# Performance work log

Hardware: AMD Instinct MI355X
Metric: run time of the kernel (lower is better)

## Reference

```python
import jax, jax.numpy as jnp
import numpy as np

N = 100000   # nodes
M = 200000   # gathered (combined-subgraph) node entries
E = 600000   # combined-subgraph edges
B = 128      # graphs
P = 32       # patches per graph (METIS)
BP = B * P
DIN = 64; H = 256; RW = 16
L = 4        # GCN layers
LM = 4       # mixer layers
T = 64       # token-mixing hidden dim
CH = 4 * H   # channel-mixing hidden dim
DOUT = 10


def _seg_mean(v, idx, n):
    s = jax.ops.segment_sum(v, idx, num_segments=n)
    c = jax.ops.segment_sum(jnp.ones((v.shape[0],), v.dtype), idx, num_segments=n)
    return s / jnp.maximum(c, 1.0)[:, None]


def _ln(x, s, b):
    m = jnp.mean(x, -1, keepdims=True)
    v = jnp.var(x, -1, keepdims=True)
    return (x - m) * jax.lax.rsqrt(v + 1e-5) * s + b


def setup_inputs() -> dict:
    key = jax.random.key(0)
    ks = jax.random.split(key, 40)
    w = lambda k, s: jax.random.normal(k, s, jnp.float32) * 0.02
    inp = {
        'x': jax.random.normal(ks[0], (N, DIN), jnp.float32),
        'patch_pe': jax.random.normal(ks[1], (BP, RW), jnp.float32),
        'mask': jnp.ones((B, P), jnp.bool_),
        'nodes_mapper': jax.random.randint(ks[2], (M,), 0, N),
        'subgraphs_batch': jnp.sort(jax.random.randint(ks[3], (M,), 0, BP)),
        'edge_index': jax.random.randint(ks[4], (2, E), 0, M),
        # pre_mp
        'W_pre': w(ks[5], (DIN, H)), 'b_pre': jnp.zeros((H,), jnp.float32),
        # U MLPs (layers-1 of them) and GCN weights
        'W_u': w(ks[6], (L - 1, H, H)), 'b_u': jnp.zeros((L - 1, H), jnp.float32),
        'W_g': w(ks[7], (L, H, H)), 'b_g': jnp.zeros((L, H), jnp.float32),
        # patch RW-PE 2-layer MLP
        'Wp1': w(ks[8], (RW, H)), 'bp1': jnp.zeros((H,), jnp.float32),
        'Wp2': w(ks[9], (H, H)), 'bp2': jnp.zeros((H,), jnp.float32),
        # MLPMixer blocks (stacked over LM layers)
        'ln1_s': jnp.ones((LM, H), jnp.float32), 'ln1_b': jnp.zeros((LM, H), jnp.float32),
        'Wt1': w(ks[10], (LM, P, T)), 'bt1': jnp.zeros((LM, T), jnp.float32),
        'Wt2': w(ks[11], (LM, T, P)), 'bt2': jnp.zeros((LM, P), jnp.float32),
        'ln2_s': jnp.ones((LM, H), jnp.float32), 'ln2_b': jnp.zeros((LM, H), jnp.float32),
        'Wc1': w(ks[12], (LM, H, CH)), 'bc1': jnp.zeros((LM, CH), jnp.float32),
        'Wc2': w(ks[13], (LM, CH, H)), 'bc2': jnp.zeros((LM, H), jnp.float32),
        # head
        'ln_f_s': jnp.ones((H,), jnp.float32), 'ln_f_b': jnp.zeros((H,), jnp.float32),
        'W_head': w(ks[14], (H, DOUT)), 'b_head': jnp.zeros((DOUT,), jnp.float32),
    }
    return inp


def reference(x, patch_pe, mask, nodes_mapper, subgraphs_batch, edge_index,
              W_pre, b_pre, W_u, b_u, W_g, b_g, Wp1, bp1, Wp2, bp2,
              ln1_s, ln1_b, Wt1, bt1, Wt2, bt2, ln2_s, ln2_b, Wc1, bc1, Wc2, bc2,
              ln_f_s, ln_f_b, W_head, b_head):
    # pre_mp: linear + relu on node features [N, H]
    h = jax.nn.relu(x @ W_pre + b_pre)
    # gather nodes into combined-subgraph space [M, H]
    h = h[nodes_mapper]
    src, dst = edge_index[0], edge_index[1]
    # GCN symmetric normalization with self loops (degree over M-space)
    deg = jax.ops.segment_sum(jnp.ones((src.shape[0],), h.dtype), dst, num_segments=M) + 1.0
    nrm = jax.lax.rsqrt(deg)
    edge_nrm = (nrm[src] * nrm[dst])[:, None]
    self_nrm = (nrm * nrm)[:, None]
    for i in range(L):
        if i > 0:
            # pre_layer_scatter: pool per subgraph, broadcast back, add U-MLP
            sub = _seg_mean(h, subgraphs_batch, BP)[subgraphs_batch]
            h = h + jax.nn.relu(sub @ W_u[i - 1] + b_u[i - 1])
            # post_layer_scatter: mean over duplicated nodes, broadcast back
            h = _seg_mean(h, nodes_mapper, N)[nodes_mapper]
        # GCNConv + relu
        hw = h @ W_g[i]
        agg = jax.ops.segment_sum(hw[src] * edge_nrm, dst, num_segments=M)
        h = jax.nn.relu(agg + hw * self_nrm + b_g[i])
    # final_scatter: pool to [B*P, H]
    h = _seg_mean(h, subgraphs_batch, BP)
    # patch random-walk PE encoder (2-layer MLP) added
    pe = jax.nn.relu(jax.nn.relu(patch_pe @ Wp1 + bp1) @ Wp2 + bp2)
    z = (h + pe).reshape(B, P, H)
    # MLPMixer
    for l in range(LM):
        y = jnp.swapaxes(_ln(z, ln1_s[l], ln1_b[l]), 1, 2)  # [B, H, P]
        y = jax.nn.gelu(y @ Wt1[l] + bt1[l]) @ Wt2[l] + bt2[l]
        z = z + jnp.swapaxes(y, 1, 2)
        y = _ln(z, ln2_s[l], ln2_b[l])
        z = z + (jax.nn.gelu(y @ Wc1[l] + bc1[l]) @ Wc2[l] + bc2[l])
    # masked mean pooling over patches
    m = mask.astype(z.dtype)
    g = (z * m[:, :, None]).sum(1) / m.sum(1, keepdims=True)
    # head
    g = _ln(g, ln_f_s, ln_f_b)
    return g @ W_head + b_head
```

## Files before the change

### kernel.cpp

```cpp
#include <hip/hip_runtime.h>
#include <math.h>

namespace {

typedef unsigned short u16;
typedef unsigned int u32;
typedef unsigned long long u64;
typedef __attribute__((ext_vector_type(8))) short bf16x8;
typedef __attribute__((ext_vector_type(8))) unsigned short u16x8;
typedef __attribute__((ext_vector_type(4))) float f32x4;

constexpr int kN = 100000, kM = 200000, kE = 600000;
constexpr int kB = 128, kP = 32, kBP = kB * kP;
constexpr int kDIN = 64, kH = 256, kRW = 16;
constexpr int kL = 4, kLM = 4, kT = 64, kCH = 4 * kH, kDOUT = 10;
constexpr int kScanCB = 1024;

__device__ __forceinline__ float geluf(float x) {
  const float c = 0.7978845608028654f;
  float x3 = x * x * x;
  return 0.5f * x * (1.f + tanhf(c * (x + 0.044715f * x3)));
}

__device__ __forceinline__ float bf2f(u16 h) {
  u32 u = ((u32)h) << 16;
  return __uint_as_float(u);
}
__device__ __forceinline__ u16 f2bf(float f) {
  u32 u = __float_as_uint(f);
  u32 r = (u + 0x7FFFu + ((u >> 16) & 1u)) >> 16;
  return (u16)r;
}
__device__ __forceinline__ float4 bf4_to_f4(ushort4 v) {
  return make_float4(bf2f(v.x), bf2f(v.y), bf2f(v.z), bf2f(v.w));
}
__device__ __forceinline__ ushort4 f4_to_bf4(float4 v) {
  ushort4 r;
  r.x = f2bf(v.x); r.y = f2bf(v.y); r.z = f2bf(v.z); r.w = f2bf(v.w);
  return r;
}

template <int RPT>
__global__ __launch_bounds__(256) void k_gemm(
    const float* __restrict__ A, const float* __restrict__ B,
    const float* __restrict__ bias, const float* __restrict__ res,
    float* __restrict__ C, int Mr, int Nc, int Kc, int act) {
  constexpr int BM = 16 * RPT;
  __shared__ float As[16][BM];
  __shared__ float Bs[16][64];
  int tid = threadIdx.x;
  int tx = tid & 15, ty = tid >> 4;
  int bm = blockIdx.x * BM, bn = blockIdx.y * 64;
  float acc[RPT][4];
#pragma unroll
  for (int i = 0; i < RPT; ++i)
#pragma unroll
    for (int j = 0; j < 4; ++j) acc[i][j] = 0.f;

  for (int k0 = 0; k0 < Kc; k0 += 16) {
#pragma unroll
    for (int l = 0; l < RPT / 4; ++l) {
      int idx = tid + l * 256;
      int r = idx >> 2, c4 = (idx & 3) * 4;
      float4 a4 = make_float4(0.f, 0.f, 0.f, 0.f);
      if (bm + r < Mr) a4 = *(const float4*)(A + (size_t)(bm + r) * Kc + k0 + c4);
      As[c4 + 0][r] = a4.x; As[c4 + 1][r] = a4.y;
      As[c4 + 2][r] = a4.z; As[c4 + 3][r] = a4.w;
    }
    {
      int kr = tid >> 4, cc = (tid & 15) * 4;
      float4 b4 = *(const float4*)(B + (size_t)(k0 + kr) * Nc + bn + cc);
      *(float4*)&Bs[kr][cc] = b4;
    }
    __syncthreads();
#pragma unroll
    for (int k = 0; k < 16; ++k) {
      float a[RPT], bb[4];
#pragma unroll
      for (int l = 0; l < RPT / 4; ++l) {
        float4 av = *(const float4*)&As[k][ty * RPT + l * 4];
        a[l * 4 + 0] = av.x; a[l * 4 + 1] = av.y;
        a[l * 4 + 2] = av.z; a[l * 4 + 3] = av.w;
      }
      float4 bv = *(const float4*)&Bs[k][tx * 4];
      bb[0] = bv.x; bb[1] = bv.y; bb[2] = bv.z; bb[3] = bv.w;
#pragma unroll
      for (int i = 0; i < RPT; ++i)
#pragma unroll
        for (int j = 0; j < 4; ++j) acc[i][j] = fmaf(a[i], bb[j], acc[i][j]);
    }
    __syncthreads();
  }
#pragma unroll
  for (int i = 0; i < RPT; ++i) {
    int row = bm + ty * RPT + i;
    if (row >= Mr) continue;
#pragma unroll
    for (int j = 0; j < 4; ++j) {
      int col = bn + tx * 4 + j;
      float v = acc[i][j];
      if (bias) v += bias[col];
      if (act == 1) v = fmaxf(v, 0.f);
      else if (act == 2) v = geluf(v);
      if (res) v += res[(size_t)row * Nc + col];
      C[(size_t)row * Nc + col] = v;
    }
  }
}

__global__ void k_packw(const float* __restrict__ W, u16* __restrict__ Wp,
                        int KB, int NC, int L) {
  int per = KB * NC * 16 * 64;
  int o8 = blockIdx.x * 256 + threadIdx.x;
  if (o8 >= L * per) return;
  int li = o8 / per, r = o8 % per;
  int l = r & 63;
  int t = r >> 6;
  int nt = t & 15, q = t >> 4;
  int kbg = q % KB, nc = q / KB;
  int Kc = KB * 32, Ncols = NC * 256;
  int col = nc * 256 + nt * 16 + (l & 15);
  int k0 = kbg * 32 + (l >> 4) * 8;
  const float* w = W + (size_t)li * Kc * Ncols;
  u16* o = Wp + (size_t)o8 * 8;
#pragma unroll
  for (int i = 0; i < 8; ++i) o[i] = f2bf(w[(size_t)(k0 + i) * Ncols + col]);
}

__global__ __launch_bounds__(256) void k_gemm_rowblk_mfma(
    const u16* A, const u16* __restrict__ Wp, u16* C, int Mr) {
  __shared__ u16 As[64 * 256];
  __shared__ u16 Bs[8192];
  int tid = threadIdx.x;
  int w = tid >> 6, l = tid & 63;
  int bm = blockIdx.x * 64;
  u16x8 pre[4];
#pragma unroll
  for (int j = 0; j < 4; ++j) pre[j] = *(const u16x8*)(Wp + tid * 8 + j * 2048);
#pragma unroll
  for (int i = 0; i < 8; ++i) {
    int idx = tid + i * 256;
    int row = idx >> 5, seg = idx & 31;
    u16x8 v = (u16x8){0, 0, 0, 0, 0, 0, 0, 0};
    if (bm + row < Mr) v = *(const u16x8*)(A + (size_t)(bm + row) * 256 + seg * 8);
    *(u16x8*)((char*)As + row * 512 + ((seg * 16) ^ ((row & 15) << 4))) = v;
  }

  f32x4 acc[16];
#pragma unroll
  for (int nt = 0; nt < 16; ++nt) acc[nt] = (f32x4){0.f, 0.f, 0.f, 0.f};
  int a_row = w * 16 + (l & 15);
  int a_xor = (a_row & 15) << 4;
  for (int kb = 0; kb < 8; ++kb) {
    __syncthreads();
#pragma unroll
    for (int j = 0; j < 4; ++j) *(u16x8*)(Bs + tid * 8 + j * 2048) = pre[j];
    __syncthreads();
    if (kb < 7) {
#pragma unroll
      for (int j = 0; j < 4; ++j)
        pre[j] = *(const u16x8*)(Wp + (kb + 1) * 8192 + tid * 8 + j * 2048);
    }
    int abyte = a_row * 512 + ((kb * 64 + (l >> 4) * 16) ^ a_xor);
    bf16x8 af = *(const bf16x8*)((const char*)As + abyte);
#pragma unroll
    for (int nt = 0; nt < 16; ++nt) {
      bf16x8 bf = *(const bf16x8*)(Bs + nt * 512 + l * 8);
      acc[nt] = __builtin_amdgcn_mfma_f32_16x16x32_bf16(af, bf, acc[nt], 0, 0, 0);
    }
  }
  __syncthreads();
  int c_row0 = w * 16 + (l >> 4) * 4;
  int ccol = l & 15;
#pragma unroll
  for (int nt = 0; nt < 16; ++nt) {
#pragma unroll
    for (int j = 0; j < 4; ++j) {
      int row = c_row0 + j;
      int colbyte = (nt * 16 + ccol) * 2;
      *(u16*)((char*)As + row * 512 + (colbyte ^ ((row & 15) << 4))) = f2bf(acc[nt][j]);
    }
  }
  __syncthreads();
#pragma unroll
  for (int i = 0; i < 8; ++i) {
    int idx = tid + i * 256;
    int row = idx >> 5, seg = idx & 31;
    if (bm + row < Mr) {
      u16x8 v = *(const u16x8*)((const char*)As + row * 512 + ((seg * 16) ^ ((row & 15) << 4)));
      *(u16x8*)(C + (size_t)(bm + row) * 256 + seg * 8) = v;
    }
  }
}

__global__ __launch_bounds__(256) void k_gemm_mfma_s(
    const void* __restrict__ Av, const u16* __restrict__ Wp,
    const float* __restrict__ bias, const float* __restrict__ res,
    void* __restrict__ Cv, int Kc, int Ncols, int act, int outw, int abf, int kclen) {
  __shared__ u16 As[64 * 256];
  __shared__ u16 Bs[8192];
  int tid = threadIdx.x;
  int w = tid >> 6, l = tid & 63;
  int bm = blockIdx.x * 64;
  int nchunk = blockIdx.y, bn = nchunk * 256;
  int kcs = blockIdx.z * kclen;
  int KB = Kc >> 5;
  const u16* wseq = Wp + (size_t)nchunk * KB * 8192;

  u16x8 pre[4];
#pragma unroll
  for (int j = 0; j < 4; ++j)
    pre[j] = *(const u16x8*)(wseq + (size_t)(kcs >> 5) * 8192 + tid * 8 + j * 2048);

  f32x4 acc[16];
#pragma unroll
  for (int nt = 0; nt < 16; ++nt) acc[nt] = (f32x4){0.f, 0.f, 0.f, 0.f};
  int a_row = w * 16 + (l & 15);
  int a_xor = (a_row & 15) << 4;

  for (int kc0 = kcs; kc0 < kcs + kclen; kc0 += 256) {
    __syncthreads();
#pragma unroll
    for (int i = 0; i < 8; ++i) {
      int idx = tid + i * 256;
      int row = idx >> 5, seg = idx & 31;
      u16x8 hv;
      if (abf) {
        hv = *(const u16x8*)((const u16*)Av + (size_t)(bm + row) * Kc + kc0 + seg * 8);
      } else {
        const float* s = (const float*)Av + (size_t)(bm + row) * Kc + kc0 + seg * 8;
        float4 v0 = *(const float4*)s;
        float4 v1 = *(const float4*)(s + 4);
        hv[0] = f2bf(v0.x); hv[1] = f2bf(v0.y); hv[2] = f2bf(v0.z); hv[3] = f2bf(v0.w);
        hv[4] = f2bf(v1.x); hv[5] = f2bf(v1.y); hv[6] = f2bf(v1.z); hv[7] = f2bf(v1.w);
      }
      *(u16x8*)((char*)As + row * 512 + ((seg * 16) ^ ((row & 15) << 4))) = hv;
    }
    int kbg0 = kc0 >> 5;
    for (int kb = 0; kb < 8; ++kb) {
      int t = kbg0 + kb;
      __syncthreads();
#pragma unroll
      for (int j = 0; j < 4; ++j) *(u16x8*)(Bs + tid * 8 + j * 2048) = pre[j];
      __syncthreads();
      if (t + 1 < KB) {
#pragma unroll
        for (int j = 0; j < 4; ++j)
          pre[j] = *(const u16x8*)(wseq + (size_t)(t + 1) * 8192 + tid * 8 + j * 2048);
      }
      int abyte = a_row * 512 + ((kb * 64 + (l >> 4) * 16) ^ a_xor);
      bf16x8 af = *(const bf16x8*)((const char*)As + abyte);
#pragma unroll
      for (int nt = 0; nt < 16; ++nt) {
        bf16x8 bf = *(const bf16x8*)(Bs + nt * 512 + l * 8);
        acc[nt] = __builtin_amdgcn_mfma_f32_16x16x32_bf16(af, bf, acc[nt], 0, 0, 0);
      }
    }
  }

  int c_row0 = w * 16 + (l >> 4) * 4;
  int ccol = l & 15;
  if (outw == 2) {
    float* C = (float*)Cv;
    bool addb = (kcs == 0);
#pragma unroll
    for (int nt = 0; nt < 16; ++nt) {
      int col = bn + nt * 16 + ccol;
      float bv = addb ? bias[col] : 0.f;
#pragma unroll
      for (int j = 0; j < 4; ++j) {
        int row = bm + c_row0 + j;
        atomicAdd(&C[(size_t)row * Ncols + col], acc[nt][j] + bv);
      }
    }
  } else if (outw == 1) {
    float* C = (float*)Cv;
#pragma unroll
    for (int nt = 0; nt < 16; ++nt) {
      int col = bn + nt * 16 + ccol;
      float bv = bias[col];
#pragma unroll
      for (int j = 0; j < 4; ++j) {
        int row = bm + c_row0 + j;
        float v = acc[nt][j] + bv;
        if (act == 1) v = fmaxf(v, 0.f);
        else if (act == 2) v = geluf(v);
        if (res) v += res[(size_t)row * Ncols + col];
        C[(size_t)row * Ncols + col] = v;
      }
    }
  } else {
    u16* C = (u16*)Cv;
    __syncthreads();
#pragma unroll
    for (int nt = 0; nt < 16; ++nt) {
      float bv = bias[bn + nt * 16 + ccol];
#pragma unroll
      for (int j = 0; j < 4; ++j) {
        int row = c_row0 + j;
        float v = acc[nt][j] + bv;
        if (act == 1) v = fmaxf(v, 0.f);
        else if (act == 2) v = geluf(v);
        int colbyte = (nt * 16 + ccol) * 2;
        *(u16*)((char*)As + row * 512 + (colbyte ^ ((row & 15) << 4))) = f2bf(v);
      }
    }
    __syncthreads();
#pragma unroll
    for (int i = 0; i < 8; ++i) {
      int idx = tid + i * 256;
      int row = idx >> 5, seg = idx & 31;
      u16x8 v = *(const u16x8*)((const char*)As + row * 512 + ((seg * 16) ^ ((row & 15) << 4)));
      *(u16x8*)(C + (size_t)(bm + row) * Ncols + bn + seg * 8) = v;
    }
  }
}

__global__ __launch_bounds__(256) void k_premp_mfma(
    const float* __restrict__ A, const u16* __restrict__ Wp,
    const float* __restrict__ bias, u16* __restrict__ C, int Mr) {
  __shared__ u16 As[64 * 256];
  __shared__ u16 Bs[8192];
  int tid = threadIdx.x;
  int w = tid >> 6, l = tid & 63;
  int bm = blockIdx.x * 64;
  u16x8 pre[4];
#pragma unroll
  for (int j = 0; j < 4; ++j) pre[j] = *(const u16x8*)(Wp + tid * 8 + j * 2048);
#pragma unroll
  for (int i = 0; i < 2; ++i) {
    int idx = tid + i * 256;
    int row = idx >> 3, seg = idx & 7;
    u16x8 hv = (u16x8){0, 0, 0, 0, 0, 0, 0, 0};
    if (bm + row < Mr) {
      const float* s = A + (size_t)(bm + row) * 64 + seg * 8;
      float4 v0 = *(const float4*)s;
      float4 v1 = *(const float4*)(s + 4);
      hv[0] = f2bf(v0.x); hv[1] = f2bf(v0.y); hv[2] = f2bf(v0.z); hv[3] = f2bf(v0.w);
      hv[4] = f2bf(v1.x); hv[5] = f2bf(v1.y); hv[6] = f2bf(v1.z); hv[7] = f2bf(v1.w);
    }
    *(u16x8*)((char*)As + row * 128 + ((seg * 16) ^ ((row & 7) << 4))) = hv;
  }

  f32x4 acc[16];
#pragma unroll
  for (int nt = 0; nt < 16; ++nt) acc[nt] = (f32x4){0.f, 0.f, 0.f, 0.f};
  int a_row = w * 16 + (l & 15);
#pragma unroll
  for (int kb = 0; kb < 2; ++kb) {
    __syncthreads();
#pragma unroll
    for (int j = 0; j < 4; ++j) *(u16x8*)(Bs + tid * 8 + j * 2048) = pre[j];
    __syncthreads();
    if (kb == 0) {
#pragma unroll
      for (int j = 0; j < 4; ++j)
        pre[j] = *(const u16x8*)(Wp + 8192 + tid * 8 + j * 2048);
    }
    int abyte = a_row * 128 + ((kb * 64 + (l >> 4) * 16) ^ ((a_row & 7) << 4));
    bf16x8 af = *(const bf16x8*)((const char*)As + abyte);
#pragma unroll
    for (int nt = 0; nt < 16; ++nt) {
      bf16x8 bf = *(const bf16x8*)(Bs + nt * 512 + l * 8);
      acc[nt] = __builtin_amdgcn_mfma_f32_16x16x32_bf16(af, bf, acc[nt], 0, 0, 0);
    }
  }
  __syncthreads();
  int c_row0 = w * 16 + (l >> 4) * 4;
  int ccol = l & 15;
#pragma unroll
  for (int nt = 0; nt < 16; ++nt) {
    float bv = bias[nt * 16 + ccol];
#pragma unroll
    for (int j = 0; j < 4; ++j) {
      int row = c_row0 + j;
      float v = fmaxf(acc[nt][j] + bv, 0.f);
      int colbyte = (nt * 16 + ccol) * 2;
      *(u16*)((char*)As + row * 512 + (colbyte ^ ((row & 15) << 4))) = f2bf(v);
    }
  }
  __syncthreads();
#pragma unroll
  for (int i = 0; i < 8; ++i) {
    int idx = tid + i * 256;
    int row = idx >> 5, seg = idx & 31;
    if (bm + row < Mr) {
      u16x8 v = *(const u16x8*)((const char*)As + row * 512 + ((seg * 16) ^ ((row & 15) << 4)));
      *(u16x8*)(C + (size_t)(bm + row) * 256 + seg * 8) = v;
    }
  }
}

__global__ void k_hist(const int* __restrict__ idx, int* __restrict__ cnt, int n) {
  int i = blockIdx.x * 256 + threadIdx.x;
  if (i < n) atomicAdd(&cnt[idx[i]], 1);
}

__global__ __launch_bounds__(256) void k_scan_a(const int* __restrict__ cnt, int n,
                                                int* __restrict__ bsum) {
  __shared__ int red[256];
  int b = blockIdx.x, t = threadIdx.x;
  int base = b * kScanCB + t * 4;
  int s = 0;
#pragma unroll
  for (int j = 0; j < 4; ++j) { int i = base + j; if (i < n) s += cnt[i]; }
  red[t] = s;
  __syncthreads();
  for (int d = 128; d; d >>= 1) {
    if (t < d) red[t] += red[t + d];
    __syncthreads();
  }
  if (t == 0) bsum[b] = red[0];
}

__global__ __launch_bounds__(256) void k_scan_b(const int* __restrict__ bsum, int G,
                                                int* __restrict__ boff,
                                                int* __restrict__ total_out) {
  __shared__ int sd[256];
  int t = threadIdx.x;
  sd[t] = (t < G) ? bsum[t] : 0;
  __syncthreads();
  for (int d = 1; d < 256; d <<= 1) {
    int u = (t >= d) ? sd[t - d] : 0;
    __syncthreads();
    sd[t] += u;
    __syncthreads();
  }
  if (t < G) boff[t] = t ? sd[t - 1] : 0;
  if (t == 255) *total_out = sd[255];
}

__global__ __launch_bounds__(256) void k_scan_c(const int* __restrict__ cnt, int n,
                                                const int* __restrict__ boff,
                                                int* __restrict__ out) {
  __shared__ int sd[256];
  int b = blockIdx.x, t = threadIdx.x;
  int base = b * kScanCB + t * 4;
  int c[4];
  int s = 0;
#pragma unroll
  for (int j = 0; j < 4; ++j) {
    int i = base + j;
    c[j] = (i < n) ? cnt[i] : 0;
    s += c[j];
  }
  sd[t] = s;
  __syncthreads();
  for (int d = 1; d < 256; d <<= 1) {
    int u = (t >= d) ? sd[t - d] : 0;
    __syncthreads();
    sd[t] += u;
    __syncthreads();
  }
  int run = boff[b] + (t ? sd[t - 1] : 0);
#pragma unroll
  for (int j = 0; j < 4; ++j) {
    int i = base + j;
    if (i < n) out[i] = run;
    run += c[j];
  }
}

__global__ void k_nrm(const int* __restrict__ cnt, float* __restrict__ nrm, int n) {
  int i = blockIdx.x * 256 + threadIdx.x;
  if (i < n) nrm[i] = rsqrtf((float)cnt[i] + 1.f);
}

__global__ void k_scatter_e(const int* __restrict__ src, const int* __restrict__ dst,
                            const int* __restrict__ nmap, const float* __restrict__ nrm,
                            const int* __restrict__ rs, int* __restrict__ cur,
                            int* __restrict__ gidx, float* __restrict__ w) {
  int e = blockIdx.x * 256 + threadIdx.x;
  if (e >= kE) return;
  int s = src[e], d = dst[e];
  int p = rs[d] + atomicAdd(&cur[d], 1);
  gidx[p] = nmap[s];
  w[p] = nrm[s] * nrm[d];
}

__global__ void k_scatter_m(const int* __restrict__ nmap, const int* __restrict__ rs,
                            int* __restrict__ cur, int* __restrict__ lst) {
  int m = blockIdx.x * 256 + threadIdx.x;
  if (m >= kM) return;
  int n = nmap[m];
  int p = rs[n] + atomicAdd(&cur[n], 1);
  lst[p] = m;
}

__global__ void k_bpstart(const int* __restrict__ sb, int* __restrict__ bps) {
  int bp = blockIdx.x * 256 + threadIdx.x;
  if (bp > kBP) return;
  if (bp == kBP) { bps[kBP] = kM; return; }
  int lo = 0, hi = kM;
  while (lo < hi) { int mid = (lo + hi) >> 1; if (sb[mid] < bp) lo = mid + 1; else hi = mid; }
  bps[bp] = lo;
}

__global__ __launch_bounds__(256) void k_pool_seg_b(const u16* __restrict__ h,
                                                    const int* __restrict__ bps,
                                                    float* __restrict__ out) {
  __shared__ float red[4][256];
  int bp = blockIdx.x;
  int tid = threadIdx.x;
  int wv = tid >> 6, lane = tid & 63;
  int lo = bps[bp], hi = bps[bp + 1];
  float4 acc = make_float4(0.f, 0.f, 0.f, 0.f);
  for (int m = lo + wv; m < hi; m += 4) {
    float4 v = bf4_to_f4(*(const ushort4*)(h + (size_t)m * 256 + lane * 4));
    acc.x += v.x; acc.y += v.y; acc.z += v.z; acc.w += v.w;
  }
  *(float4*)&red[wv][lane * 4] = acc;
  __syncthreads();
  float s = red[0][tid] + red[1][tid] + red[2][tid] + red[3][tid];
  out[(size_t)bp * kH + tid] = s / fmaxf((float)(hi - lo), 1.f);
}

__global__ __launch_bounds__(256) void k_pool_n_f(const u16* __restrict__ h,
                                                  const float* __restrict__ ub,
                                                  const int* __restrict__ sb,
                                                  const int* __restrict__ rs,
                                                  const int* __restrict__ lst,
                                                  u16* __restrict__ outp) {
  int wv = threadIdx.x >> 6, lane = threadIdx.x & 63;
  int n = blockIdx.x * 4 + wv;
  if (n >= kN) return;
  int lo = rs[n], hi = rs[n + 1];
  float4 acc = make_float4(0.f, 0.f, 0.f, 0.f);
  for (int p = lo; p < hi; p += 2) {
    int p1 = min(p + 1, hi - 1);
    int m0 = lst[p], m1 = lst[p1];
    float c1 = (p + 1 < hi) ? 1.f : 0.f;
    float4 v0 = bf4_to_f4(*(const ushort4*)(h + (size_t)m0 * 256 + lane * 4));
    float4 v1 = bf4_to_f4(*(const ushort4*)(h + (size_t)m1 * 256 + lane * 4));
    float4 u0 = ((const float4*)ub)[(size_t)sb[m0] * 64 + lane];
    float4 u1 = ((const float4*)ub)[(size_t)sb[m1] * 64 + lane];
    acc.x += v0.x + u0.x + c1 * (v1.x + u1.x);
    acc.y += v0.y + u0.y + c1 * (v1.y + u1.y);
    acc.z += v0.z + u0.z + c1 * (v1.z + u1.z);
    acc.w += v0.w + u0.w + c1 * (v1.w + u1.w);
  }
  float inv = 1.f / fmaxf((float)(hi - lo), 1.f);
  acc.x *= inv; acc.y *= inv; acc.z *= inv; acc.w *= inv;
  *(ushort4*)(outp + (size_t)n * 256 + lane * 4) = f4_to_bf4(acc);
}

__global__ __launch_bounds__(256) void k_gcn_b(const u16* __restrict__ hw,
                                               const int* __restrict__ nmap,
                                               const float* __restrict__ nrm,
                                               const int* __restrict__ rs,
                                               const int* __restrict__ gidx,
                                               const float* __restrict__ w,
                                               const float* __restrict__ bias,
                                               u16* __restrict__ outp) {
  int wv = threadIdx.x >> 6, lane = threadIdx.x & 63;
  int m = blockIdx.x * 4 + wv;
  if (m >= kM) return;
  float nm_ = nrm[m];
  float sn = nm_ * nm_;
  float4 b4 = ((const float4*)bias)[lane];
  float4 sv = bf4_to_f4(*(const ushort4*)(hw + (size_t)nmap[m] * 256 + lane * 4));
  float4 acc;
  acc.x = fmaf(sv.x, sn, b4.x); acc.y = fmaf(sv.y, sn, b4.y);
  acc.z = fmaf(sv.z, sn, b4.z); acc.w = fmaf(sv.w, sn, b4.w);
  int lo = rs[m], hi = rs[m + 1];
  for (int p0 = lo; p0 < hi; p0 += 4) {
    int last = hi - 1;
    int q1 = min(p0 + 1, last), q2 = min(p0 + 2, last), q3 = min(p0 + 3, last);
    int g0 = gidx[p0], g1 = gidx[q1], g2 = gidx[q2], g3 = gidx[q3];
    float w0 = w[p0];
    float w1 = (p0 + 1 < hi) ? w[q1] : 0.f;
    float w2 = (p0 + 2 < hi) ? w[q2] : 0.f;
    float w3 = (p0 + 3 < hi) ? w[q3] : 0.f;
    float4 v0 = bf4_to_f4(*(const ushort4*)(hw + (size_t)g0 * 256 + lane * 4));
    float4 v1 = bf4_to_f4(*(const ushort4*)(hw + (size_t)g1 * 256 + lane * 4));
    float4 v2 = bf4_to_f4(*(const ushort4*)(hw + (size_t)g2 * 256 + lane * 4));
    float4 v3 = bf4_to_f4(*(const ushort4*)(hw + (size_t)g3 * 256 + lane * 4));
    acc.x = fmaf(v3.x, w3, fmaf(v2.x, w2, fmaf(v1.x, w1, fmaf(v0.x, w0, acc.x))));
    acc.y = fmaf(v3.y, w3, fmaf(v2.y, w2, fmaf(v1.y, w1, fmaf(v0.y, w0, acc.y))));
    acc.z = fmaf(v3.z, w3, fmaf(v2.z, w2, fmaf(v1.z, w1, fmaf(v0.z, w0, acc.z))));
    acc.w = fmaf(v3.w, w3, fmaf(v2.w, w2, fmaf(v1.w, w1, fmaf(v0.w, w0, acc.w))));
  }
  acc.x = fmaxf(acc.x, 0.f); acc.y = fmaxf(acc.y, 0.f);
  acc.z = fmaxf(acc.z, 0.f); acc.w = fmaxf(acc.w, 0.f);
  *(ushort4*)(outp + (size_t)m * 256 + lane * 4) = f4_to_bf4(acc);
}

__global__ __launch_bounds__(256) void k_ln(const float* __restrict__ x,
                                            const float* __restrict__ s,
                                            const float* __restrict__ b,
                                            float* __restrict__ y) {
  __shared__ float t1[4], t2[4];
  int r = blockIdx.x, j = threadIdx.x;
  float v = x[(size_t)r * kH + j];
  float a = v, q = v * v;
  for (int o = 32; o; o >>= 1) { a += __shfl_down(a, o, 64); q += __shfl_down(q, o, 64); }
  if ((j & 63) == 0) { t1[j >> 6] = a; t2[j >> 6] = q; }
  __syncthreads();
  float sum = t1[0] + t1[1] + t1[2] + t1[3];
  float sq = t2[0] + t2[1] + t2[2] + t2[3];
  float mu = sum * (1.f / 256.f);
  float var = sq * (1.f / 256.f) - mu * mu;
  y[(size_t)r * kH + j] = (v - mu) * rsqrtf(var + 1e-5f) * s[j] + b[j];
}

__global__ __launch_bounds__(256) void k_token(const float* __restrict__ zn,
                                               const float* __restrict__ Wt1,
                                               const float* __restrict__ bt1,
                                               const float* __restrict__ Wt2,
                                               const float* __restrict__ bt2,
                                               float* __restrict__ z) {
  __shared__ float zs[32][65];
  __shared__ float w1[32][64];
  __shared__ float w2[64][33];
  __shared__ float y1[64][65];
  int bb = blockIdx.x, hb = blockIdx.y * 64;
  int t = threadIdx.x;
  for (int i = t; i < 2048; i += 256) {
    int p = i >> 6, hh = i & 63;
    zs[p][hh] = zn[((size_t)bb * 32 + p) * kH + hb + hh];
  }
  for (int i = t; i < 2048; i += 256) { int p = i >> 6, tt = i & 63; w1[p][tt] = Wt1[p * 64 + tt]; }
  for (int i = t; i < 2048; i += 256) { int tt = i >> 5, p = i & 31; w2[tt][p] = Wt2[tt * 32 + p]; }
  __syncthreads();
  for (int i = t; i < 4096; i += 256) {
    int hh = i >> 6, tt = i & 63;
    float a = bt1[tt];
#pragma unroll
    for (int p = 0; p < 32; ++p) a = fmaf(zs[p][hh], w1[p][tt], a);
    y1[hh][tt] = geluf(a);
  }
  __syncthreads();
  for (int i = t; i < 2048; i += 256) {
    int hh = i >> 5, p = i & 31;
    float a = bt2[p];
#pragma unroll
    for (int tt = 0; tt < 64; ++tt) a = fmaf(y1[hh][tt], w2[tt][p], a);
    z[((size_t)bb * 32 + p) * kH + hb + hh] += a;
  }
}

__global__ void k_gpool(const float* __restrict__ z, float* __restrict__ g) {
  int bb = blockIdx.x, j = threadIdx.x;
  float s = 0.f;
  for (int p = 0; p < 32; ++p) s += z[((size_t)bb * 32 + p) * kH + j];
  g[bb * kH + j] = s * (1.f / 32.f);
}

__global__ __launch_bounds__(256) void k_head(const float* __restrict__ g,
                                              const float* __restrict__ s,
                                              const float* __restrict__ b,
                                              const float* __restrict__ Wh,
                                              const float* __restrict__ bh,
                                              float* __restrict__ out) {
  __shared__ float t1[4], t2[4];
  __shared__ float row[256];
  int bb = blockIdx.x, j = threadIdx.x;
  float v = g[bb * kH + j];
  float a = v, q = v * v;
  for (int o = 32; o; o >>= 1) { a += __shfl_down(a, o, 64); q += __shfl_down(q, o, 64); }
  if ((j & 63) == 0) { t1[j >> 6] = a; t2[j >> 6] = q; }
  __syncthreads();
  float sum = t1[0] + t1[1] + t1[2] + t1[3];
  float sq = t2[0] + t2[1] + t2[2] + t2[3];
  float mu = sum * (1.f / 256.f);
  float var = sq * (1.f / 256.f) - mu * mu;
  row[j] = (v - mu) * rsqrtf(var + 1e-5f) * s[j] + b[j];
  __syncthreads();
  if (j < kDOUT) {
    float acc = bh[j];
    for (int k = 0; k < kH; ++k) acc = fmaf(row[k], Wh[k * kDOUT + j], acc);
    out[bb * kDOUT + j] = acc;
  }
}

}

extern "C" void kernel_launch(void* const* d_in, const int* in_sizes, int n_in,
                              void* d_out, int out_size, void* d_ws, size_t ws_size,
                              hipStream_t stream) {
  const float* x = (const float*)d_in[0];
  const float* ppe = (const float*)d_in[1];
  const int* nmap = (const int*)d_in[3];
  const int* sb = (const int*)d_in[4];
  const int* esrc = (const int*)d_in[5];
  const int* edst = esrc + kE;
  const float* Wpre = (const float*)d_in[6];
  const float* bpre = (const float*)d_in[7];
  const float* Wu = (const float*)d_in[8];
  const float* bu = (const float*)d_in[9];
  const float* Wg = (const float*)d_in[10];
  const float* bg = (const float*)d_in[11];
  const float* Wp1 = (const float*)d_in[12];
  const float* bp1 = (const float*)d_in[13];
  const float* Wp2 = (const float*)d_in[14];
  const float* bp2 = (const float*)d_in[15];
  const float* ln1s = (const float*)d_in[16];
  const float* ln1b = (const float*)d_in[17];
  const float* Wt1 = (const float*)d_in[18];
  const float* bt1 = (const float*)d_in[19];
  const float* Wt2 = (const float*)d_in[20];
  const float* bt2 = (const float*)d_in[21];
  const float* ln2s = (const float*)d_in[22];
  const float* ln2b = (const float*)d_in[23];
  const float* Wc1 = (const float*)d_in[24];
  const float* bc1 = (const float*)d_in[25];
  const float* Wc2 = (const float*)d_in[26];
  const float* bc2 = (const float*)d_in[27];
  const float* lnfs = (const float*)d_in[28];
  const float* lnfb = (const float*)d_in[29];
  const float* Whd = (const float*)d_in[30];
  const float* bhd = (const float*)d_in[31];
  float* out = (float*)d_out;

  u16* h_M = (u16*)d_ws;
  u16* h_N = h_M + (size_t)kM * kH;
  float* sub = (float*)(h_N + (size_t)kN * kH);
  float* ubuf = sub + (size_t)kBP * kH;
  float* csrw = ubuf + (size_t)kBP * kH;
  float* nrm = csrw + kE;
  int* rsE = (int*)(nrm + kM);
  int* gidx = rsE + kM + 1;
  int* rsN = gidx + kE;
  int* mlst = rsN + kN + 1;
  int* cntE = mlst + kM;
  int* cntN = cntE + kM;
  int* bps = cntN + kN;
  int* bsumS = bps + kBP + 1;
  int* boffS = bsumS + 256;
  size_t need = ((size_t)(boffS + 256)) - ((size_t)d_ws);
  if (ws_size < need) {
    hipMemsetAsync(d_out, 0, (size_t)out_size * sizeof(float), stream);
    return;
  }

  u16* wpackG = (u16*)(((size_t)cntE + 15) & ~(size_t)15);
  u16* wpackPre = wpackG + 4 * 65536;
  u16* wpackU = wpackPre + 16384;

  float* z = (float*)d_ws;
  float* zn = z + (size_t)kBP * kH;
  float* c1 = zn + (size_t)kBP * kH;
  float* g = c1 + (size_t)kBP * kCH;
  u16* wpackC = (u16*)(g + kB * kH);
  u16* wpackC2 = wpackC + 4 * 262144;
  u16* wpackP2 = wpackC2 + 4 * 262144;

  hipMemsetAsync(cntE, 0, kM * sizeof(int), stream);
  hipMemsetAsync(cntN, 0, kN * sizeof(int), stream);

  constexpr int GscanM = (kM + kScanCB - 1) / kScanCB;
  constexpr int GscanN = (kN + kScanCB - 1) / kScanCB;

  k_hist<<<(kE + 255) / 256, 256, 0, stream>>>(edst, cntE, kE);
  k_hist<<<(kM + 255) / 256, 256, 0, stream>>>(nmap, cntN, kM);
  k_scan_a<<<GscanM, 256, 0, stream>>>(cntE, kM, bsumS);
  k_scan_b<<<1, 256, 0, stream>>>(bsumS, GscanM, boffS, rsE + kM);
  k_scan_c<<<GscanM, 256, 0, stream>>>(cntE, kM, boffS, rsE);
  k_scan_a<<<GscanN, 256, 0, stream>>>(cntN, kN, bsumS);
  k_scan_b<<<1, 256, 0, stream>>>(bsumS, GscanN, boffS, rsN + kN);
  k_scan_c<<<GscanN, 256, 0, stream>>>(cntN, kN, boffS, rsN);
  k_nrm<<<(kM + 255) / 256, 256, 0, stream>>>(cntE, nrm, kM);
  hipMemsetAsync(cntE, 0, kM * sizeof(int), stream);
  hipMemsetAsync(cntN, 0, kN * sizeof(int), stream);
  k_scatter_e<<<(kE + 255) / 256, 256, 0, stream>>>(esrc, edst, nmap, nrm, rsE, cntE, gidx, csrw);
  k_scatter_m<<<(kM + 255) / 256, 256, 0, stream>>>(nmap, rsN, cntN, mlst);
  k_bpstart<<<(kBP + 256) / 256, 256, 0, stream>>>(sb, bps);
  k_packw<<<(4 * 8192 + 255) / 256, 256, 0, stream>>>(Wg, wpackG, 8, 1, 4);
  k_packw<<<(2048 + 255) / 256, 256, 0, stream>>>(Wpre, wpackPre, 2, 1, 1);
  k_packw<<<(3 * 8192 + 255) / 256, 256, 0, stream>>>(Wu, wpackU, 8, 1, 3);

  k_premp_mfma<<<(kN + 63) / 64, 256, 0, stream>>>(x, wpackPre, bpre, h_N, kN);

  for (int i = 0; i < kL; ++i) {
    if (i > 0) {
      k_pool_seg_b<<<kBP, 256, 0, stream>>>(h_M, bps, sub);
      k_gemm_mfma_s<<<dim3(64, 1), 256, 0, stream>>>(
          sub, wpackU + (size_t)(i - 1) * 65536, bu + (i - 1) * kH, nullptr,
          ubuf, 256, 256, 1, 1, 0, 256);
      k_pool_n_f<<<(kN + 3) / 4, 256, 0, stream>>>(h_M, ubuf, sb, rsN, mlst, h_N);
    }
    k_gemm_rowblk_mfma<<<(kN + 63) / 64, 256, 0, stream>>>(
        h_N, wpackG + (size_t)i * 65536, h_N, kN);
    k_gcn_b<<<(kM + 3) / 4, 256, 0, stream>>>(h_N, nmap, nrm, rsE, gidx, csrw, bg + i * kH, h_M);
  }

  k_pool_seg_b<<<kBP, 256, 0, stream>>>(h_M, bps, sub);
  k_packw<<<(4 * 32768 + 255) / 256, 256, 0, stream>>>(Wc1, wpackC, 8, 4, 4);
  k_packw<<<(4 * 32768 + 255) / 256, 256, 0, stream>>>(Wc2, wpackC2, 32, 1, 4);
  k_packw<<<(8192 + 255) / 256, 256, 0, stream>>>(Wp2, wpackP2, 8, 1, 1);

  dim3 gBP4((kBP + 63) / 64, kH / 64);
  k_gemm<4><<<gBP4, 256, 0, stream>>>(ppe, Wp1, bp1, nullptr, ubuf, kBP, kH, kRW, 1);
  k_gemm_mfma_s<<<dim3(64, 1), 256, 0, stream>>>(ubuf, wpackP2, bp2, sub, z,
                                                 256, 256, 1, 1, 0, 256);

  for (int l = 0; l < kLM; ++l) {
    k_ln<<<kBP, 256, 0, stream>>>(z, ln1s + l * kH, ln1b + l * kH, zn);
    dim3 gt(kB, kH / 64);
    k_token<<<gt, 256, 0, stream>>>(zn, Wt1 + l * kP * kT, bt1 + l * kT,
                                    Wt2 + l * kT * kP, bt2 + l * kP, z);
    k_ln<<<kBP, 256, 0, stream>>>(z, ln2s + l * kH, ln2b + l * kH, zn);
    k_gemm_mfma_s<<<dim3(64, 4), 256, 0, stream>>>(
        zn, wpackC + (size_t)l * 262144, bc1 + l * kCH, nullptr,
        (u16*)c1, 256, 1024, 2, 0, 0, 256);
    k_gemm_mfma_s<<<dim3(64, 1, 4), 256, 0, stream>>>(
        (const u16*)c1, wpackC2 + (size_t)l * 262144, bc2 + l * kH, nullptr,
        z, 1024, 256, 0, 2, 1, 256);
  }

  k_gpool<<<kB, 256, 0, stream>>>(z, g);
  k_head<<<kB, 256, 0, stream>>>(g, lnfs, lnfb, Whd, bhd, out);
}
```

Before: 1.206 ms.

## Process two rows per wave in gather kernels and fuse preprocessing launches

The GCN aggregation and node-pooling kernels now give each wavefront two consecutive output rows, walking their joint CSR range with a wider unroll (8 for GCN, 4 for pooling) so more gather loads are in flight at once. The two histogram launches are merged into one, the norm computation moves into the scan kernel, and the paired memsets are combined into single calls. This cuts per-row loop overhead and launch count, at the cost of branchy split handling at the row boundary, more registers per thread, and grid sizes that assume kM and kN are divisible by 8. It also relies on cntE and cntN being contiguous, which a single memset covering both now assumes.

New measurement: 1.292 ms. 7.1% more time.

```diff
diff --git a/kernel.cpp b/kernel.cpp
--- a/kernel.cpp
+++ b/kernel.cpp
@@ -391,9 +391,14 @@
   }
 }
 
-__global__ void k_hist(const int* __restrict__ idx, int* __restrict__ cnt, int n) {
+__global__ void k_hist2(const int* __restrict__ edst, const int* __restrict__ nmap,
+                        int* __restrict__ cntE, int* __restrict__ cntN) {
   int i = blockIdx.x * 256 + threadIdx.x;
-  if (i < n) atomicAdd(&cnt[idx[i]], 1);
+  if (i < kE) {
+    atomicAdd(&cntE[edst[i]], 1);
+  } else if (i < kE + kM) {
+    atomicAdd(&cntN[nmap[i - kE]], 1);
+  }
 }
 
 __global__ __launch_bounds__(256) void k_scan_a(const int* __restrict__ cnt, int n,
@@ -432,7 +437,8 @@
 
 __global__ __launch_bounds__(256) void k_scan_c(const int* __restrict__ cnt, int n,
                                                 const int* __restrict__ boff,
-                                                int* __restrict__ out) {
+                                                int* __restrict__ out,
+                                                float* __restrict__ nrmOut) {
   __shared__ int sd[256];
   int b = blockIdx.x, t = threadIdx.x;
   int base = b * kScanCB + t * 4;
@@ -456,14 +462,12 @@
 #pragma unroll
   for (int j = 0; j < 4; ++j) {
     int i = base + j;
-    if (i < n) out[i] = run;
+    if (i < n) {
+      out[i] = run;
+      if (nrmOut) nrmOut[i] = rsqrtf((float)c[j] + 1.f);
+    }
     run += c[j];
   }
-}
-
-__global__ void k_nrm(const int* __restrict__ cnt, float* __restrict__ nrm, int n) {
-  int i = blockIdx.x * 256 + threadIdx.x;
-  if (i < n) nrm[i] = rsqrtf((float)cnt[i] + 1.f);
 }
 
 __global__ void k_scatter_e(const int* __restrict__ src, const int* __restrict__ dst,
@@ -522,26 +526,52 @@
                                                   const int* __restrict__ lst,
                                                   u16* __restrict__ outp) {
   int wv = threadIdx.x >> 6, lane = threadIdx.x & 63;
-  int n = blockIdx.x * 4 + wv;
-  if (n >= kN) return;
-  int lo = rs[n], hi = rs[n + 1];
-  float4 acc = make_float4(0.f, 0.f, 0.f, 0.f);
-  for (int p = lo; p < hi; p += 2) {
-    int p1 = min(p + 1, hi - 1);
-    int m0 = lst[p], m1 = lst[p1];
-    float c1 = (p + 1 < hi) ? 1.f : 0.f;
-    float4 v0 = bf4_to_f4(*(const ushort4*)(h + (size_t)m0 * 256 + lane * 4));
-    float4 v1 = bf4_to_f4(*(const ushort4*)(h + (size_t)m1 * 256 + lane * 4));
-    float4 u0 = ((const float4*)ub)[(size_t)sb[m0] * 64 + lane];
-    float4 u1 = ((const float4*)ub)[(size_t)sb[m1] * 64 + lane];
-    acc.x += v0.x + u0.x + c1 * (v1.x + u1.x);
-    acc.y += v0.y + u0.y + c1 * (v1.y + u1.y);
-    acc.z += v0.z + u0.z + c1 * (v1.z + u1.z);
-    acc.w += v0.w + u0.w + c1 * (v1.w + u1.w);
-  }
-  float inv = 1.f / fmaxf((float)(hi - lo), 1.f);
-  acc.x *= inv; acc.y *= inv; acc.z *= inv; acc.w *= inv;
-  *(ushort4*)(outp + (size_t)n * 256 + lane * 4) = f4_to_bf4(acc);
+  int n0 = blockIdx.x * 8 + wv * 2;
+  int lo0 = rs[n0], hi0 = rs[n0 + 1], hi1 = rs[n0 + 2];
+  float4 acc0 = make_float4(0.f, 0.f, 0.f, 0.f);
+  float4 acc1 = make_float4(0.f, 0.f, 0.f, 0.f);
+  for (int p = lo0; p < hi1; p += 4) {
+    int last = hi1 - 1;
+    float4 v[4];
+    float wj[4];
+#pragma unroll
+    for (int j = 0; j < 4; ++j) {
+      int pp = min(p + j, last);
+      int m = lst[pp];
+      float4 hv = bf4_to_f4(*(const ushort4*)(h + (size_t)m * 256 + lane * 4));
+      float4 uv = ((const float4*)ub)[(size_t)sb[m] * 64 + lane];
+      v[j] = make_float4(hv.x + uv.x, hv.y + uv.y, hv.z + uv.z, hv.w + uv.w);
+      wj[j] = (p + j < hi1) ? 1.f : 0.f;
+    }
+    if (p + 3 < hi0) {
+#pragma unroll
+      for (int j = 0; j < 4; ++j) {
+        acc0.x += v[j].x; acc0.y += v[j].y; acc0.z += v[j].z; acc0.w += v[j].w;
+      }
+    } else if (p >= hi0) {
+#pragma unroll
+      for (int j = 0; j < 4; ++j) {
+        acc1.x = fmaf(v[j].x, wj[j], acc1.x); acc1.y = fmaf(v[j].y, wj[j], acc1.y);
+        acc1.z = fmaf(v[j].z, wj[j], acc1.z); acc1.w = fmaf(v[j].w, wj[j], acc1.w);
+      }
+    } else {
+#pragma unroll
+      for (int j = 0; j < 4; ++j) {
+        float wa = (p + j < hi0) ? wj[j] : 0.f;
+        float wb = wj[j] - wa;
+        acc0.x = fmaf(v[j].x, wa, acc0.x); acc0.y = fmaf(v[j].y, wa, acc0.y);
+        acc0.z = fmaf(v[j].z, wa, acc0.z); acc0.w = fmaf(v[j].w, wa, acc0.w);
+        acc1.x = fmaf(v[j].x, wb, acc1.x); acc1.y = fmaf(v[j].y, wb, acc1.y);
+        acc1.z = fmaf(v[j].z, wb, acc1.z); acc1.w = fmaf(v[j].w, wb, acc1.w);
+      }
+    }
+  }
+  float i0 = 1.f / fmaxf((float)(hi0 - lo0), 1.f);
+  float i1 = 1.f / fmaxf((float)(hi1 - hi0), 1.f);
+  acc0.x *= i0; acc0.y *= i0; acc0.z *= i0; acc0.w *= i0;
+  acc1.x *= i1; acc1.y *= i1; acc1.z *= i1; acc1.w *= i1;
+  *(ushort4*)(outp + (size_t)n0 * 256 + lane * 4) = f4_to_bf4(acc0);
+  *(ushort4*)(outp + (size_t)(n0 + 1) * 256 + lane * 4) = f4_to_bf4(acc1);
 }
 
 __global__ __launch_bounds__(256) void k_gcn_b(const u16* __restrict__ hw,
@@ -553,36 +583,60 @@
                                                const float* __restrict__ bias,
                                                u16* __restrict__ outp) {
   int wv = threadIdx.x >> 6, lane = threadIdx.x & 63;
-  int m = blockIdx.x * 4 + wv;
-  if (m >= kM) return;
-  float nm_ = nrm[m];
-  float sn = nm_ * nm_;
+  int m0 = blockIdx.x * 8 + wv * 2;
+  int m1 = m0 + 1;
+  float na = nrm[m0], nb = nrm[m1];
+  float sa = na * na, sbv = nb * nb;
   float4 b4 = ((const float4*)bias)[lane];
-  float4 sv = bf4_to_f4(*(const ushort4*)(hw + (size_t)nmap[m] * 256 + lane * 4));
-  float4 acc;
-  acc.x = fmaf(sv.x, sn, b4.x); acc.y = fmaf(sv.y, sn, b4.y);
-  acc.z = fmaf(sv.z, sn, b4.z); acc.w = fmaf(sv.w, sn, b4.w);
-  int lo = rs[m], hi = rs[m + 1];
-  for (int p0 = lo; p0 < hi; p0 += 4) {
-    int last = hi - 1;
-    int q1 = min(p0 + 1, last), q2 = min(p0 + 2, last), q3 = min(p0 + 3, last);
-    int g0 = gidx[p0], g1 = gidx[q1], g2 = gidx[q2], g3 = gidx[q3];
-    float w0 = w[p0];
-    float w1 = (p0 + 1 < hi) ? w[q1] : 0.f;
-    float w2 = (p0 + 2 < hi) ? w[q2] : 0.f;
-    float w3 = (p0 + 3 < hi) ? w[q3] : 0.f;
-    float4 v0 = bf4_to_f4(*(const ushort4*)(hw + (size_t)g0 * 256 + lane * 4));
-    float4 v1 = bf4_to_f4(*(const ushort4*)(hw + (size_t)g1 * 256 + lane * 4));
-    float4 v2 = bf4_to_f4(*(const ushort4*)(hw + (size_t)g2 * 256 + lane * 4));
-    float4 v3 = bf4_to_f4(*(const ushort4*)(hw + (size_t)g3 * 256 + lane * 4));
-    acc.x = fmaf(v3.x, w3, fmaf(v2.x, w2, fmaf(v1.x, w1, fmaf(v0.x, w0, acc.x))));
-    acc.y = fmaf(v3.y, w3, fmaf(v2.y, w2, fmaf(v1.y, w1, fmaf(v0.y, w0, acc.y))));
-    acc.z = fmaf(v3.z, w3, fmaf(v2.z, w2, fmaf(v1.z, w1, fmaf(v0.z, w0, acc.z))));
-    acc.w = fmaf(v3.w, w3, fmaf(v2.w, w2, fmaf(v1.w, w1, fmaf(v0.w, w0, acc.w))));
-  }
-  acc.x = fmaxf(acc.x, 0.f); acc.y = fmaxf(acc.y, 0.f);
-  acc.z = fmaxf(acc.z, 0.f); acc.w = fmaxf(acc.w, 0.f);
-  *(ushort4*)(outp + (size_t)m * 256 + lane * 4) = f4_to_bf4(acc);
+  float4 s0 = bf4_to_f4(*(const ushort4*)(hw + (size_t)nmap[m0] * 256 + lane * 4));
+  float4 s1 = bf4_to_f4(*(const ushort4*)(hw + (size_t)nmap[m1] * 256 + lane * 4));
+  float4 acc0, acc1;
+  acc0.x = fmaf(s0.x, sa, b4.x); acc0.y = fmaf(s0.y, sa, b4.y);
+  acc0.z = fmaf(s0.z, sa, b4.z); acc0.w = fmaf(s0.w, sa, b4.w);
+  acc1.x = fmaf(s1.x, sbv, b4.x); acc1.y = fmaf(s1.y, sbv, b4.y);
+  acc1.z = fmaf(s1.z, sbv, b4.z); acc1.w = fmaf(s1.w, sbv, b4.w);
+  int lo0 = rs[m0], hi0 = rs[m1], hi1 = rs[m1 + 1];
+  for (int p = lo0; p < hi1; p += 8) {
+    int last = hi1 - 1;
+    float4 v[8];
+    float wj[8];
+#pragma unroll
+    for (int j = 0; j < 8; ++j) {
+      int pp = min(p + j, last);
+      int gi = gidx[pp];
+      wj[j] = (p + j < hi1) ? w[pp] : 0.f;
+      v[j] = bf4_to_f4(*(const ushort4*)(hw + (size_t)gi * 256 + lane * 4));
+    }
+    if (p + 7 < hi0) {
+#pragma unroll
+      for (int j = 0; j < 8; ++j) {
+        acc0.x = fmaf(v[j].x, wj[j], acc0.x); acc0.y = fmaf(v[j].y, wj[j], acc0.y);
+        acc0.z = fmaf(v[j].z, wj[j], acc0.z); acc0.w = fmaf(v[j].w, wj[j], acc0.w);
+      }
+    } else if (p >= hi0) {
+#pragma unroll
+      for (int j = 0; j < 8; ++j) {
+        acc1.x = fmaf(v[j].x, wj[j], acc1.x); acc1.y = fmaf(v[j].y, wj[j], acc1.y);
+        acc1.z = fmaf(v[j].z, wj[j], acc1.z); acc1.w = fmaf(v[j].w, wj[j], acc1.w);
+      }
+    } else {
+#pragma unroll
+      for (int j = 0; j < 8; ++j) {
+        float wa = (p + j < hi0) ? wj[j] : 0.f;
+        float wb = wj[j] - wa;
+        acc0.x = fmaf(v[j].x, wa, acc0.x); acc0.y = fmaf(v[j].y, wa, acc0.y);
+        acc0.z = fmaf(v[j].z, wa, acc0.z); acc0.w = fmaf(v[j].w, wa, acc0.w);
+        acc1.x = fmaf(v[j].x, wb, acc1.x); acc1.y = fmaf(v[j].y, wb, acc1.y);
+        acc1.z = fmaf(v[j].z, wb, acc1.z); acc1.w = fmaf(v[j].w, wb, acc1.w);
+      }
+    }
+  }
+  acc0.x = fmaxf(acc0.x, 0.f); acc0.y = fmaxf(acc0.y, 0.f);
+  acc0.z = fmaxf(acc0.z, 0.f); acc0.w = fmaxf(acc0.w, 0.f);
+  acc1.x = fmaxf(acc1.x, 0.f); acc1.y = fmaxf(acc1.y, 0.f);
+  acc1.z = fmaxf(acc1.z, 0.f); acc1.w = fmaxf(acc1.w, 0.f);
+  *(ushort4*)(outp + (size_t)m0 * 256 + lane * 4) = f4_to_bf4(acc0);
+  *(ushort4*)(outp + (size_t)m1 * 256 + lane * 4) = f4_to_bf4(acc1);
 }
 
 __global__ __launch_bounds__(256) void k_ln(const float* __restrict__ x,
@@ -745,23 +799,19 @@
   u16* wpackC2 = wpackC + 4 * 262144;
   u16* wpackP2 = wpackC2 + 4 * 262144;
 
-  hipMemsetAsync(cntE, 0, kM * sizeof(int), stream);
-  hipMemsetAsync(cntN, 0, kN * sizeof(int), stream);
+  hipMemsetAsync(cntE, 0, (kM + kN) * sizeof(int), stream);
 
   constexpr int GscanM = (kM + kScanCB - 1) / kScanCB;
   constexpr int GscanN = (kN + kScanCB - 1) / kScanCB;
 
-  k_hist<<<(kE + 255) / 256, 256, 0, stream>>>(edst, cntE, kE);
-  k_hist<<<(kM + 255) / 256, 256, 0, stream>>>(nmap, cntN, kM);
+  k_hist2<<<(kE + kM + 255) / 256, 256, 0, stream>>>(edst, nmap, cntE, cntN);
   k_scan_a<<<GscanM, 256, 0, stream>>>(cntE, kM, bsumS);
   k_scan_b<<<1, 256, 0, stream>>>(bsumS, GscanM, boffS, rsE + kM);
-  k_scan_c<<<GscanM, 256, 0, stream>>>(cntE, kM, boffS, rsE);
+  k_scan_c<<<GscanM, 256, 0, stream>>>(cntE, kM, boffS, rsE, nrm);
   k_scan_a<<<GscanN, 256, 0, stream>>>(cntN, kN, bsumS);
   k_scan_b<<<1, 256, 0, stream>>>(bsumS, GscanN, boffS, rsN + kN);
-  k_scan_c<<<GscanN, 256, 0, stream>>>(cntN, kN, boffS, rsN);
-  k_nrm<<<(kM + 255) / 256, 256, 0, stream>>>(cntE, nrm, kM);
-  hipMemsetAsync(cntE, 0, kM * sizeof(int), stream);
-  hipMemsetAsync(cntN, 0, kN * sizeof(int), stream);
+  k_scan_c<<<GscanN, 256, 0, stream>>>(cntN, kN, boffS, rsN, nullptr);
+  hipMemsetAsync(cntE, 0, (kM + kN) * sizeof(int), stream);
   k_scatter_e<<<(kE + 255) / 256, 256, 0, stream>>>(esrc, edst, nmap, nrm, rsE, cntE, gidx, csrw);
   k_scatter_m<<<(kM + 255) / 256, 256, 0, stream>>>(nmap, rsN, cntN, mlst);
   k_bpstart<<<(kBP + 256) / 256, 256, 0, stream>>>(sb, bps);
@@ -777,11 +827,11 @@
       k_gemm_mfma_s<<<dim3(64, 1), 256, 0, stream>>>(
           sub, wpackU + (size_t)(i - 1) * 65536, bu + (i - 1) * kH, nullptr,
           ubuf, 256, 256, 1, 1, 0, 256);
-      k_pool_n_f<<<(kN + 3) / 4, 256, 0, stream>>>(h_M, ubuf, sb, rsN, mlst, h_N);
+      k_pool_n_f<<<kN / 8, 256, 0, stream>>>(h_M, ubuf, sb, rsN, mlst, h_N);
     }
     k_gemm_rowblk_mfma<<<(kN + 63) / 64, 256, 0, stream>>>(
         h_N, wpackG + (size_t)i * 65536, h_N, kN);
-    k_gcn_b<<<(kM + 3) / 4, 256, 0, stream>>>(h_N, nmap, nrm, rsE, gidx, csrw, bg + i * kH, h_M);
+    k_gcn_b<<<kM / 8, 256, 0, stream>>>(h_N, nmap, nrm, rsE, gidx, csrw, bg + i * kH, h_M);
   }
 
   k_pool_seg_b<<<kBP, 256, 0, stream>>>(h_M, bps, sub);
```
